# Optimization experiments

Hardware: AMD Instinct MI355X
Metric: run time of the kernel (lower is better)

The kernel has to match this reference:

```python
import jax, jax.numpy as jnp
import numpy as np
from jax import lax

B, C, H, G = 128, 512, 14, 20  # batch, channels, feature-map size, num branches

# landmark indices for (point1, point2) of the 10 regions, and y-offset coefficients (x ruler)
_I1 = jnp.array([21, 18, 19, 41, 38, 49, 48, 51, 61, 56])
_I2 = jnp.array([22, 25, 24, 46, 43, 53, 54, 57, 63, 58])
_COEF = jnp.array([-0.5, -1.0 / 3.0, 1.0 / 3.0, 1.0, 0.0, 0.0, 0.0, 0.0, 0.0, 0.5], jnp.float32)


def process_landmarks(y):
    # y: [B,68,2] (x,y) pixel coords -> region_array [B,10,4] = (x1,y1,x2,y2)/16
    xl, yl = y[:, :, 0], y[:, :, 1]
    ruler = jnp.abs(xl[:, 39] - xl[:, 42])            # [B]
    off = ruler[:, None] * _COEF[None, :]             # [B,10]
    region = jnp.stack([xl[:, _I1], yl[:, _I1] + off, xl[:, _I2], yl[:, _I2] + off], axis=-1)
    return region / 16.0


def _crop(xi, cyi, cxi):
    # xi: [C,H,W]; 3x3 window centered at (cyi, cxi)
    z = jnp.asarray(0, cyi.dtype)
    return lax.dynamic_slice(xi, (z, cyi - 1, cxi - 1), (C, 3, 3))


def setup_inputs() -> dict:
    key = jax.random.key(0)
    ks = jax.random.split(key, 4)
    x = jax.random.normal(ks[0], (B, C, H, H), jnp.float32)
    y = jax.random.uniform(ks[1], (B, 68, 2), jnp.float32) * 224.0
    conv_w = jax.random.normal(ks[2], (G * C, C, 3, 3), jnp.float32) * 0.02  # grouped OIHW
    conv_b = jnp.zeros((G * C,), jnp.float32)
    fc_w = jax.random.normal(ks[3], (G, C * 36, 150), jnp.float32) * 0.01
    fc_b = jnp.zeros((G, 150), jnp.float32)
    return {"x": x, "y": y, "conv_w": conv_w, "conv_b": conv_b, "fc_w": fc_w, "fc_b": fc_b}


def reference(x, y, conv_w, conv_b, fc_w, fc_b):
    bsz = x.shape[0]
    pos = jnp.clip(process_landmarks(y).astype(jnp.int32), 1, 12)   # [B,10,4]
    cx = pos[:, :, jnp.array([0, 2])].reshape(bsz, G)               # [B,20] cols
    cy = pos[:, :, jnp.array([1, 3])].reshape(bsz, G)               # [B,20] rows
    crops = jax.vmap(jax.vmap(_crop, in_axes=(None, 0, 0)), in_axes=(0, 0, 0))(x, cy, cx)  # [B,20,C,3,3]
    new_input = crops.reshape(bsz, G * C, 3, 3)
    up = jax.image.resize(new_input, (bsz, G * C, 6, 6), method='bilinear')  # half-pixel, matches torch align_corners=False
    conv = lax.conv_general_dilated(up, conv_w, (1, 1), ((1, 1), (1, 1)),
                                    feature_group_count=G,
                                    dimension_numbers=('NCHW', 'OIHW', 'NCHW'))
    conv = jax.nn.relu(conv + conv_b[None, :, None, None])          # [B, G*C, 6, 6]
    feat = conv.reshape(bsz, G, C * 36)
    fc = jax.nn.relu(jnp.einsum('bgi,gio->bgo', feat, fc_w) + fc_b[None])  # [B,G,150]
    return fc.reshape(bsz, G * 150)
```

## Files before the change

### kernel.cpp

```cpp
#include <hip/hip_runtime.h>
#include <stdint.h>

#define B_  128
#define C_  512
#define G_  20
#define K2  4608
#define FCK 18432

typedef unsigned short u16;
typedef unsigned int   u32;
typedef __attribute__((ext_vector_type(8))) short  short8;
typedef __attribute__((ext_vector_type(4))) float  float4v;

__device__ __forceinline__ u16 f2bf(float f) {
  u32 u = __builtin_bit_cast(u32, f);
  u = (u + 0x7fffu + ((u >> 16) & 1u)) >> 16;
  return (u16)u;
}

__device__ __forceinline__ void load_lds16(const void* g, void* l) {
  __builtin_amdgcn_global_load_lds(
      (const __attribute__((address_space(1))) void*)(uintptr_t)g,
      (__attribute__((address_space(3))) void*)(uint32_t)(uintptr_t)l,
      16, 0, 0);
}

#define BAR() __builtin_amdgcn_s_barrier()

__global__ void k_pos(const float* __restrict__ y, int* __restrict__ cx, int* __restrict__ cy) {
  int b = blockIdx.x * blockDim.x + threadIdx.x;
  if (b >= B_) return;
  const int   I1[10] = {21,18,19,41,38,49,48,51,61,56};
  const int   I2[10] = {22,25,24,46,43,53,54,57,63,58};
  const float CF[10] = {-0.5f, -1.0f/3.0f, 1.0f/3.0f, 1.0f, 0.f,0.f,0.f,0.f,0.f, 0.5f};
  const float* yb = y + b * 136;
  float ruler = fabsf(yb[2*39] - yb[2*42]);
  for (int j = 0; j < 10; ++j) {
    float off = ruler * CF[j];
    float vx1 = yb[2*I1[j]];
    float vy1 = yb[2*I1[j]+1] + off;
    float vx2 = yb[2*I2[j]];
    float vy2 = yb[2*I2[j]+1] + off;
    int px1 = (int)(vx1 * 0.0625f); px1 = min(max(px1,1),12);
    int py1 = (int)(vy1 * 0.0625f); py1 = min(max(py1,1),12);
    int px2 = (int)(vx2 * 0.0625f); px2 = min(max(px2,1),12);
    int py2 = (int)(vy2 * 0.0625f); py2 = min(max(py2,1),12);
    cx[b*20 + 2*j]   = px1;  cx[b*20 + 2*j+1] = px2;
    cy[b*20 + 2*j]   = py1;  cy[b*20 + 2*j+1] = py2;
  }
}

__global__ void k_convw(const float* __restrict__ w, u16* __restrict__ wb) {
  int tid = blockIdx.x * 256 + threadIdx.x;
  int o = tid >> 9, ci = tid & 511;
  const float* src = w + (size_t)tid * 9;
  u16* dst = wb + (size_t)o * K2 + ci;
  #pragma unroll
  for (int t = 0; t < 9; ++t) dst[t*512] = f2bf(src[t]);
}

__global__ void __launch_bounds__(256) k_fcw(const float* __restrict__ fw, u16* __restrict__ wfcb) {
  __shared__ u16 tile[128 * 161];
  int chunk = blockIdx.x;
  int g     = blockIdx.y;
  int tid   = threadIdx.x;
  const float* src = fw + (size_t)g * FCK * 150 + (size_t)chunk * 128 * 150;
  #pragma unroll
  for (int it = 0; it < 75; ++it) {
    int f = it * 256 + tid;
    int il = f / 150, o = f - il * 150;
    tile[il * 161 + o] = f2bf(src[f]);
  }
  __syncthreads();
  size_t dstbase = (size_t)g * 160 * FCK + (size_t)chunk * 128;
  #pragma unroll
  for (int it = 0; it < 10; ++it) {
    int wi = it * 256 + tid;
    int o = wi >> 4, il8 = (wi & 15) * 8;
    u16 vals[8];
    if (o < 150) {
      #pragma unroll
      for (int j = 0; j < 8; ++j) vals[j] = tile[(il8 + j) * 161 + o];
    } else {
      #pragma unroll
      for (int j = 0; j < 8; ++j) vals[j] = 0;
    }
    *(short8*)(wfcb + dstbase + (size_t)o * FCK + il8) = *(short8*)vals;
  }
}

__global__ void __launch_bounds__(256) k_up3(const float* __restrict__ x,
                                             const int* __restrict__ cx,
                                             const int* __restrict__ cy,
                                             u16* __restrict__ up3) {
  __shared__ float crop[3][3][C_];
  int bg = blockIdx.x;
  int b = bg / 20, g = bg % 20;
  int X = cx[bg] - 1, Y = cy[bg] - 1;
  const float* xb = x + (size_t)b * (C_*14*14);
  int t = threadIdx.x;
  for (int it = 0; it < 6; ++it) {
    int idx = it*256 + t;
    int r = idx >> 9, ci = idx & 511;
    const float* srow = xb + ci*196 + (Y + r)*14 + X;
    crop[r][0][ci] = srow[0];
    crop[r][1][ci] = srow[1];
    crop[r][2][ci] = srow[2];
  }
  __syncthreads();
  const int   R0[6] = {0,0,0,1,1,1};
  const float WA[6] = {1.f, .75f, .25f, .75f, .25f, 0.f};
  u16* dstbase = up3 + ((size_t)g*B_ + b) * 64 * C_;
  for (int it = 0; it < 16; ++it) {
    int cidx = it*256 + t;
    int pp = cidx >> 6;
    int c8 = (cidx & 63) * 8;
    int ph = pp >> 3, pw = pp & 7;
    u16 outv[8];
    if (ph == 0 || ph == 7 || pw == 0 || pw == 7) {
      #pragma unroll
      for (int j = 0; j < 8; ++j) outv[j] = 0;
    } else {
      int oh = ph - 1, ow = pw - 1;
      int r0 = R0[oh]; float wy0 = WA[oh], wy1 = 1.f - WA[oh];
      int s0 = R0[ow]; float wx0 = WA[ow], wx1 = 1.f - WA[ow];
      #pragma unroll
      for (int j = 0; j < 8; ++j) {
        int ci = c8 + j;
        float v = wy0*(wx0*crop[r0][s0][ci]   + wx1*crop[r0][s0+1][ci])
                + wy1*(wx0*crop[r0+1][s0][ci] + wx1*crop[r0+1][s0+1][ci]);
        outv[j] = f2bf(v);
      }
    }
    *(short8*)(dstbase + (size_t)pp*C_ + c8) = *(short8*)outv;
  }
}

__global__ void __launch_bounds__(512, 2) k_conv(const u16* __restrict__ wb,
                                                 const u16* __restrict__ up3,
                                                 const float* __restrict__ conv_b,
                                                 u16* __restrict__ feat) {
  __shared__ __align__(16) u16 As[2 * 256 * 64];
  __shared__ __align__(16) u16 Bs[2 * 256 * 64];
  int bid = blockIdx.x;
  int lid = (bid & 7) * 90 + (bid >> 3);
  int mt = lid & 1;
  int nt = (lid >> 1) % 18;
  int g  = lid / 36;
  int tid = threadIdx.x;
  int lane = tid & 63;
  int w = tid >> 6;
  int wr = w >> 2, wc = w & 3;
  int l15 = lane & 15, l4 = lane >> 4;

  int rl0 = tid >> 3, sl0 = tid & 7;
  const u16* srcA0 = wb + (size_t)(g*512 + mt*256 + rl0) * K2 + (sl0 ^ (rl0 & 7)) * 8;
  const u16* srcB[2][2];
  #pragma unroll
  for (int h = 0; h < 2; ++h)
    #pragma unroll
    for (int j = 0; j < 2; ++j) {
      int rl = j * 64 + rl0;
      int n  = nt * 256 + h * 128 + rl;
      unsigned bb = (unsigned)n / 36u;
      unsigned pix = (unsigned)n % 36u;
      int pixA = (int)(pix / 6u) * 8 + (int)(pix % 6u);
      srcB[h][j] = up3 + (((size_t)g*B_ + bb)*64 + pixA) * C_ + (sl0 ^ (rl0 & 7)) * 8;
    }

  auto stageA = [&](int st, int h) {
    if (st >= 72) return;
    int db = st & 1;
    size_t ko = (size_t)st * 64;
    #pragma unroll
    for (int j = 0; j < 2; ++j)
      load_lds16(srcA0 + (size_t)(h*128 + j*64) * K2 + ko,
                 (char*)As + db*32768 + h*16384 + (j*512 + tid)*16);
  };
  auto stageB = [&](int st, int h) {
    if (st >= 72) return;
    int db = st & 1;
    int t9 = st >> 3;
    size_t ko = (size_t)((t9/3)*8 + (t9%3)) * C_ + (size_t)(st & 7) * 64;
    #pragma unroll
    for (int j = 0; j < 2; ++j)
      load_lds16(srcB[h][j] + ko,
                 (char*)Bs + db*32768 + h*16384 + (j*512 + tid)*16);
  };

  auto ldfrag = [&](const char* base, int row, int kb) -> short8 {
    int cb = (kb*64 + l4*16) ^ ((row & 7) << 4);
    return *(const short8*)(base + row*128 + cb);
  };

  float4v acc[8][4];
  #pragma unroll
  for (int mi = 0; mi < 8; ++mi)
    #pragma unroll
    for (int nj = 0; nj < 4; ++nj) acc[mi][nj] = (float4v){0.f,0.f,0.f,0.f};

  stageB(0,0); stageB(0,1); stageA(0,0); stageA(0,1);
  stageB(1,0); stageB(1,1); stageA(1,0); stageA(1,1);
  asm volatile("s_waitcnt vmcnt(8)" ::: "memory");
  BAR();

  short8 aF[4][2], b01[2][2], b23[2][2];

#define LDA_HALF(BASE, MH)                                        \
  _Pragma("unroll") for (int mi = 0; mi < 4; ++mi)                \
    _Pragma("unroll") for (int kb = 0; kb < 2; ++kb)              \
      aF[mi][kb] = ldfrag(BASE, wr*128 + ((MH)*4 + mi)*16 + l15, kb);
#define LDB_HALF(BASE, NH, DST)                                   \
  _Pragma("unroll") for (int nj = 0; nj < 2; ++nj)                \
    _Pragma("unroll") for (int kb = 0; kb < 2; ++kb)              \
      DST[nj][kb] = ldfrag(BASE, wc*64 + ((NH)*2 + nj)*16 + l15, kb);
#define MFMA_QUAD(BF, QM, QN)                                     \
  __builtin_amdgcn_s_setprio(1);                                  \
  _Pragma("unroll") for (int kb = 0; kb < 2; ++kb)                \
    _Pragma("unroll") for (int mi = 0; mi < 4; ++mi)              \
      _Pragma("unroll") for (int nj = 0; nj < 2; ++nj)            \
        acc[(QM)*4+mi][(QN)*2+nj] = __builtin_amdgcn_mfma_f32_16x16x32_bf16( \
            aF[mi][kb], BF[nj][kb], acc[(QM)*4+mi][(QN)*2+nj], 0, 0, 0);     \
  __builtin_amdgcn_s_setprio(0);

  for (int it = 0; it < 36; ++it) {
    int t0 = 2 * it;
    const char* A0 = (const char*)As;
    const char* B0 = (const char*)Bs;
    const char* A1 = (const char*)As + 32768;
    const char* B1 = (const char*)Bs + 32768;
    LDA_HALF(A0, 0); LDB_HALF(B0, 0, b01);
    BAR(); MFMA_QUAD(b01, 0, 0); BAR();
    LDB_HALF(B0, 1, b23);
    BAR(); MFMA_QUAD(b23, 0, 1); BAR();
    LDA_HALF(A0, 1);
    stageB(t0 + 2, 0);
    BAR(); MFMA_QUAD(b01, 1, 0); BAR();
    stageB(t0 + 2, 1); stageA(t0 + 2, 0);
    BAR(); MFMA_QUAD(b23, 1, 1);
    if (it < 35) { asm volatile("s_waitcnt vmcnt(6)" ::: "memory"); }
    else         { asm volatile("s_waitcnt vmcnt(0)" ::: "memory"); }
    BAR();
    LDA_HALF(A1, 0); LDB_HALF(B1, 0, b01);
    stageA(t0 + 2, 1);
    BAR(); MFMA_QUAD(b01, 0, 0); BAR();
    LDB_HALF(B1, 1, b23);
    BAR(); MFMA_QUAD(b23, 0, 1); BAR();
    LDA_HALF(A1, 1);
    stageB(t0 + 3, 0);
    BAR(); MFMA_QUAD(b01, 1, 0); BAR();
    stageB(t0 + 3, 1); stageA(t0 + 3, 0); stageA(t0 + 3, 1);
    BAR(); MFMA_QUAD(b23, 1, 1);
    asm volatile("s_waitcnt vmcnt(8)" ::: "memory");
    BAR();
  }
#undef LDA_HALF
#undef LDB_HALF
#undef MFMA_QUAD

  float bias[8][4];
  #pragma unroll
  for (int mi = 0; mi < 8; ++mi)
    #pragma unroll
    for (int r = 0; r < 4; ++r)
      bias[mi][r] = conv_b[g*512 + mt*256 + wr*128 + mi*16 + l4*4 + r];
  #pragma unroll
  for (int nj = 0; nj < 4; ++nj) {
    int n = nt*256 + wc*64 + nj*16 + l15;
    unsigned bb = (unsigned)n / 36u;
    unsigned pix = (unsigned)n % 36u;
    size_t base = ((size_t)g*B_ + bb)*FCK + pix;
    #pragma unroll
    for (int mi = 0; mi < 8; ++mi)
      #pragma unroll
      for (int r = 0; r < 4; ++r) {
        int m = mt*256 + wr*128 + mi*16 + l4*4 + r;
        float v = fmaxf(acc[mi][nj][r] + bias[mi][r], 0.f);
        feat[base + (size_t)m*36] = f2bf(v);
      }
  }
}

__global__ void __launch_bounds__(256) k_fc(const u16* __restrict__ feat,
                                            const u16* __restrict__ wfcb,
                                            float* __restrict__ accum) {
  __shared__ __align__(16) u16 As[128*64];
  __shared__ __align__(16) u16 Bs[160*64];
  int sp = blockIdx.x;
  int g  = blockIdx.y;
  int tid = threadIdx.x;
  int lane = tid & 63, w = tid >> 6;
  int wr = w >> 1, wc = w & 1;
  int rl = lane >> 3, s = lane & 7;
  int l15 = lane & 15, l4 = lane >> 4;

  const u16* gA[4]; u16* lA[4];
  #pragma unroll
  for (int i = 0; i < 4; ++i) {
    int r = w*32 + i*8 + rl;
    int c = s ^ (r & 7);
    gA[i] = feat + ((size_t)g*B_ + r)*FCK + c*8;
    lA[i] = (u16*)As + (w*32 + i*8) * 64;
  }
  const u16* gB[5]; u16* lB[5];
  #pragma unroll
  for (int i = 0; i < 5; ++i) {
    int r = w*40 + i*8 + rl;
    int c = s ^ (r & 7);
    gB[i] = wfcb + ((size_t)(g*160 + r))*FCK + c*8;
    lB[i] = (u16*)Bs + (w*40 + i*8) * 64;
  }

  float4v acc[4][5];
  #pragma unroll
  for (int mi = 0; mi < 4; ++mi)
    #pragma unroll
    for (int nj = 0; nj < 5; ++nj) acc[mi][nj] = (float4v){0.f,0.f,0.f,0.f};

  size_t kbase = (size_t)sp * 1152;
  for (int stp = 0; stp < 18; ++stp) {
    size_t kofs = kbase + (size_t)stp * 64;
    __syncthreads();
    #pragma unroll
    for (int i = 0; i < 4; ++i) load_lds16(gA[i] + kofs, lA[i]);
    #pragma unroll
    for (int i = 0; i < 5; ++i) load_lds16(gB[i] + kofs, lB[i]);
    __syncthreads();

    short8 a[4][2], bf[5][2];
    #pragma unroll
    for (int kb = 0; kb < 2; ++kb) {
      #pragma unroll
      for (int mi = 0; mi < 4; ++mi) {
        int row = wr*64 + mi*16 + l15;
        int cb  = (kb*64 + l4*16) ^ ((row & 7) << 4);
        a[mi][kb] = *(const short8*)((const char*)As + row*128 + cb);
      }
      #pragma unroll
      for (int nj = 0; nj < 5; ++nj) {
        int row = wc*80 + nj*16 + l15;
        int cb  = (kb*64 + l4*16) ^ ((row & 7) << 4);
        bf[nj][kb] = *(const short8*)((const char*)Bs + row*128 + cb);
      }
    }
    #pragma unroll
    for (int kb = 0; kb < 2; ++kb)
      #pragma unroll
      for (int mi = 0; mi < 4; ++mi)
        #pragma unroll
        for (int nj = 0; nj < 5; ++nj)
          acc[mi][nj] = __builtin_amdgcn_mfma_f32_16x16x32_bf16(
              a[mi][kb], bf[nj][kb], acc[mi][nj], 0, 0, 0);
  }

  #pragma unroll
  for (int mi = 0; mi < 4; ++mi)
    #pragma unroll
    for (int r = 0; r < 4; ++r) {
      int brow = wr*64 + mi*16 + l4*4 + r;
      #pragma unroll
      for (int nj = 0; nj < 5; ++nj) {
        int o = wc*80 + nj*16 + l15;
        atomicAdd(&accum[((size_t)brow*20 + g)*160 + o], acc[mi][nj][r]);
      }
    }
}

__global__ void k_final(const float* __restrict__ accum, const float* __restrict__ fcb,
                        float* __restrict__ out) {
  int idx = blockIdx.x * 256 + threadIdx.x;
  if (idx >= B_*3000) return;
  unsigned b = (unsigned)idx / 3000u;
  unsigned rem = (unsigned)idx % 3000u;
  unsigned g = rem / 150u, o = rem % 150u;
  out[idx] = fmaxf(accum[((size_t)b*20 + g)*160 + o] + fcb[g*150 + o], 0.f);
}

extern "C" void kernel_launch(void* const* d_in, const int* in_sizes, int n_in,
                              void* d_out, int out_size, void* d_ws, size_t ws_size,
                              hipStream_t stream) {
  const float* x      = (const float*)d_in[0];
  const float* y      = (const float*)d_in[1];
  const float* conv_w = (const float*)d_in[2];
  const float* conv_b = (const float*)d_in[3];
  const float* fc_w   = (const float*)d_in[4];
  const float* fc_b   = (const float*)d_in[5];
  float* out = (float*)d_out;

  char* ws = (char*)d_ws;
  size_t off = 0;
  u16* Wb   = (u16*)(ws + off); off += (size_t)10240 * K2 * 2;
  u16* up3  = (u16*)(ws + off); off += (size_t)G_ * B_ * 64 * C_ * 2;
  u16* feat = (u16*)(ws + off); off += (size_t)G_ * B_ * FCK * 2;
  float* accum = (float*)(ws + off); off += (size_t)B_ * G_ * 160 * 4;
  int* cx = (int*)(ws + off); off += B_ * G_ * 4;
  int* cy = (int*)(ws + off); off += B_ * G_ * 4;
  u16* Wfcb = up3;

  k_pos<<<1, 128, 0, stream>>>(y, cx, cy);
  k_convw<<<(10240*512)/256, 256, 0, stream>>>(conv_w, Wb);
  k_up3<<<B_*G_, 256, 0, stream>>>(x, cx, cy, up3);
  hipMemsetAsync(accum, 0, (size_t)B_ * G_ * 160 * 4, stream);
  k_conv<<<720, 512, 0, stream>>>(Wb, up3, conv_b, feat);
  k_fcw<<<dim3(144, 20), 256, 0, stream>>>(fc_w, Wfcb);
  k_fc<<<dim3(16, 20), 256, 0, stream>>>(feat, Wfcb, accum);
  k_final<<<(B_*3000 + 255)/256, 256, 0, stream>>>(accum, fc_b, out);
}
```

Measured before the change: 629.1 us.

## Fuse FC weight bf16 conversion into FC GEMM and coalesce conv weight repack

Drops the separate k_fcw pass. The FC GEMM now reads fp32 fc_w directly, converts it to bf16 and stores it transposed into swizzled LDS, and the split-K count doubles from 16 to 32 to add blocks. The conv weight repack now reads fp32 with coalesced float4 loads and transposes through LDS so it can write 16-byte vectors. In exchange, each FC block does strided scalar global loads of fc_w and extra conversion work inside the GEMM loop, and more partial sums are accumulated.

```diff
diff --git a/kernel.cpp b/kernel.cpp
--- a/kernel.cpp
+++ b/kernel.cpp
@@ -10,6 +10,7 @@
 typedef unsigned short u16;
 typedef unsigned int   u32;
 typedef __attribute__((ext_vector_type(8))) short  short8;
+typedef __attribute__((ext_vector_type(4))) short  short4v;
 typedef __attribute__((ext_vector_type(4))) float  float4v;
 
 __device__ __forceinline__ u16 f2bf(float f) {
@@ -50,42 +51,29 @@
   }
 }
 
-__global__ void k_convw(const float* __restrict__ w, u16* __restrict__ wb) {
-  int tid = blockIdx.x * 256 + threadIdx.x;
-  int o = tid >> 9, ci = tid & 511;
-  const float* src = w + (size_t)tid * 9;
-  u16* dst = wb + (size_t)o * K2 + ci;
-  #pragma unroll
-  for (int t = 0; t < 9; ++t) dst[t*512] = f2bf(src[t]);
-}
-
-__global__ void __launch_bounds__(256) k_fcw(const float* __restrict__ fw, u16* __restrict__ wfcb) {
-  __shared__ u16 tile[128 * 161];
-  int chunk = blockIdx.x;
-  int g     = blockIdx.y;
-  int tid   = threadIdx.x;
-  const float* src = fw + (size_t)g * FCK * 150 + (size_t)chunk * 128 * 150;
-  #pragma unroll
-  for (int it = 0; it < 75; ++it) {
-    int f = it * 256 + tid;
-    int il = f / 150, o = f - il * 150;
-    tile[il * 161 + o] = f2bf(src[f]);
+__global__ void __launch_bounds__(256) k_convw(const float* __restrict__ w, u16* __restrict__ wb) {
+  __shared__ u16 lds[4 * 4608];
+  int ob = blockIdx.x * 4;
+  int tid = threadIdx.x;
+  const float4* in4 = (const float4*)(w + (size_t)ob * 4608);
+  #pragma unroll
+  for (int r = 0; r < 18; ++r) {
+    int fi = r * 256 + tid;
+    float4 v = in4[fi];
+    u16 q[4] = { f2bf(v.x), f2bf(v.y), f2bf(v.z), f2bf(v.w) };
+    *(short4v*)&lds[fi * 4] = *(short4v*)q;
   }
   __syncthreads();
-  size_t dstbase = (size_t)g * 160 * FCK + (size_t)chunk * 128;
-  #pragma unroll
-  for (int it = 0; it < 10; ++it) {
-    int wi = it * 256 + tid;
-    int o = wi >> 4, il8 = (wi & 15) * 8;
+  #pragma unroll
+  for (int r = 0; r < 9; ++r) {
+    int wi = r * 256 + tid;
+    int ci0 = (wi & 63) * 8;
+    int t   = (wi >> 6) % 9;
+    int o   = wi / 576;
     u16 vals[8];
-    if (o < 150) {
-      #pragma unroll
-      for (int j = 0; j < 8; ++j) vals[j] = tile[(il8 + j) * 161 + o];
-    } else {
-      #pragma unroll
-      for (int j = 0; j < 8; ++j) vals[j] = 0;
-    }
-    *(short8*)(wfcb + dstbase + (size_t)o * FCK + il8) = *(short8*)vals;
+    #pragma unroll
+    for (int j = 0; j < 8; ++j) vals[j] = lds[o * 4608 + (ci0 + j) * 9 + t];
+    *(short8*)(wb + ((size_t)(ob + o)) * K2 + t * 512 + ci0) = *(short8*)vals;
   }
 }
 
@@ -282,7 +270,7 @@
 }
 
 __global__ void __launch_bounds__(256) k_fc(const u16* __restrict__ feat,
-                                            const u16* __restrict__ wfcb,
+                                            const float* __restrict__ fw,
                                             float* __restrict__ accum) {
   __shared__ __align__(16) u16 As[128*64];
   __shared__ __align__(16) u16 Bs[160*64];
@@ -302,14 +290,6 @@
     gA[i] = feat + ((size_t)g*B_ + r)*FCK + c*8;
     lA[i] = (u16*)As + (w*32 + i*8) * 64;
   }
-  const u16* gB[5]; u16* lB[5];
-  #pragma unroll
-  for (int i = 0; i < 5; ++i) {
-    int r = w*40 + i*8 + rl;
-    int c = s ^ (r & 7);
-    gB[i] = wfcb + ((size_t)(g*160 + r))*FCK + c*8;
-    lB[i] = (u16*)Bs + (w*40 + i*8) * 64;
-  }
 
   float4v acc[4][5];
   #pragma unroll
@@ -317,14 +297,28 @@
     #pragma unroll
     for (int nj = 0; nj < 5; ++nj) acc[mi][nj] = (float4v){0.f,0.f,0.f,0.f};
 
-  size_t kbase = (size_t)sp * 1152;
-  for (int stp = 0; stp < 18; ++stp) {
-    size_t kofs = kbase + (size_t)stp * 64;
+  int kbase = sp * 576;
+  for (int stp = 0; stp < 9; ++stp) {
+    int i0 = kbase + stp * 64;
     __syncthreads();
     #pragma unroll
-    for (int i = 0; i < 4; ++i) load_lds16(gA[i] + kofs, lA[i]);
-    #pragma unroll
-    for (int i = 0; i < 5; ++i) load_lds16(gB[i] + kofs, lB[i]);
+    for (int i = 0; i < 4; ++i) load_lds16(gA[i] + i0, lA[i]);
+    #pragma unroll
+    for (int bit = 0; bit < 5; ++bit) {
+      int idx = bit * 256 + tid;
+      int il8 = idx / 160;
+      int o   = idx - il8 * 160;
+      u16 vals[8];
+      if (o < 150) {
+        const float* src = fw + ((size_t)g * FCK + i0 + il8 * 8) * 150 + o;
+        #pragma unroll
+        for (int j = 0; j < 8; ++j) vals[j] = f2bf(src[(size_t)j * 150]);
+      } else {
+        #pragma unroll
+        for (int j = 0; j < 8; ++j) vals[j] = 0;
+      }
+      *(short8*)((char*)Bs + o * 128 + ((il8 ^ (o & 7)) * 16)) = *(short8*)vals;
+    }
     __syncthreads();
 
     short8 a[4][2], bf[5][2];
@@ -395,14 +389,12 @@
   float* accum = (float*)(ws + off); off += (size_t)B_ * G_ * 160 * 4;
   int* cx = (int*)(ws + off); off += B_ * G_ * 4;
   int* cy = (int*)(ws + off); off += B_ * G_ * 4;
-  u16* Wfcb = up3;
 
   k_pos<<<1, 128, 0, stream>>>(y, cx, cy);
-  k_convw<<<(10240*512)/256, 256, 0, stream>>>(conv_w, Wb);
+  k_convw<<<2560, 256, 0, stream>>>(conv_w, Wb);
   k_up3<<<B_*G_, 256, 0, stream>>>(x, cx, cy, up3);
   hipMemsetAsync(accum, 0, (size_t)B_ * G_ * 160 * 4, stream);
   k_conv<<<720, 512, 0, stream>>>(Wb, up3, conv_b, feat);
-  k_fcw<<<dim3(144, 20), 256, 0, stream>>>(fc_w, Wfcb);
-  k_fc<<<dim3(16, 20), 256, 0, stream>>>(feat, Wfcb, accum);
+  k_fc<<<dim3(32, 20), 256, 0, stream>>>(feat, fc_w, accum);
   k_final<<<(B_*3000 + 255)/256, 256, 0, stream>>>(accum, fc_b, out);
 }
```

Measured after the change: 615.8 us. 2.1% less time.
